# Kernel tuning notes

Hardware: AMD Instinct MI355X
Metric: run time of the kernel (lower is better)

The kernel has to match this reference:

```python
import jax, jax.numpy as jnp
import numpy as np

NUM_COMPONENTS = 8   # component ids 1..8 present; 0 = background (excluded, as in ids[ids>0])
SMOOTH = 1e-5


def setup_inputs() -> dict:
    key = jax.random.key(0)
    k1, k2, k3 = jax.random.split(key, 3)
    B, H, W, D = 2, 160, 160, 160
    y_pred = jax.random.normal(k1, (B, 2, H, W, D), dtype=jnp.float32)
    y = jax.random.randint(k2, (B, 1, H, W, D), 0, 2).astype(jnp.int64)
    components = jax.random.randint(k3, (B, H, W, D), 0, NUM_COMPONENTS + 1).astype(jnp.int64)
    return {"y_pred": y_pred, "y": y, "components": components}


def _soft_dice_loss(inter, psum, tsum):
    # metric(masked_pred, masked_true, mask) = 1 - 2*sum(p*t)/(sum(p)+sum(t)), smoothed
    return 1.0 - (2.0 * inter + SMOOTH) / (psum + tsum + SMOOTH)


def reference(y_pred, y, components):
    # activation: softmax over channel dim 1 (binary logits)
    probs = jax.nn.softmax(y_pred, axis=1)                       # [B,2,H,W,D]
    # one-hot encode int labels -> [B,2,H,W,D] float
    true = jax.nn.one_hot(y[:, 0], y_pred.shape[1], axis=1, dtype=probs.dtype)
    B = probs.shape[0]
    V = components.shape[1] * components.shape[2] * components.shape[3]
    comp = components.reshape(B, V)
    # per-voxel channel-summed quantities (mask-multiply then reduce == segment reduce)
    pp = (probs * true).sum(axis=1).reshape(B, V)                # sum_c p*t
    sp = probs.sum(axis=1).reshape(B, V)                         # sum_c p
    st = true.sum(axis=1).reshape(B, V)                          # sum_c t
    cnt = jnp.ones((B, V), dtype=probs.dtype)

    def seg(d):
        return jax.vmap(lambda dd, cc: jax.ops.segment_sum(dd, cc, num_segments=NUM_COMPONENTS + 1))(d, comp)

    inter, psum, tsum, counts = seg(pp), seg(sp), seg(st), seg(cnt)
    # drop background (component id 0), as torch loops only over ids > 0
    inter, psum, tsum, counts = inter[:, 1:], psum[:, 1:], tsum[:, 1:], counts[:, 1:]
    dice = _soft_dice_loss(inter, psum, tsum)                    # [B, K]
    present = (counts > 0).astype(dice.dtype)                    # only ids in torch.unique
    per_sample = (dice * present).sum(axis=1) / jnp.maximum(present.sum(axis=1), 1.0)
    return per_sample.mean()
```

## Files before the change

kernel.cpp:

```cpp
#include <hip/hip_runtime.h>

#define NB 2
#define NCK 8
#define NVAL (NCK * 2)
#define NBINS (NB * NVAL)
#define SMOOTHF 1e-5f
#define MAXBLK 2048

__global__ __launch_bounds__(256) void cc_accum(
        const float* __restrict__ y_pred,
        const int* __restrict__ y,
        const int* __restrict__ comp,
        float* __restrict__ partial,
        int V4, int half, int nblk) {
    const int b   = (blockIdx.x >= half) ? 1 : 0;
    const int blk = blockIdx.x - b * half;
    const int stride = half * 256;

    float acc[NVAL];
    #pragma unroll
    for (int i = 0; i < NVAL; ++i) acc[i] = 0.0f;

    const float* p0 = y_pred + (long long)b * 2 * ((long long)V4 * 4);
    const float* p1 = p0 + (long long)V4 * 4;
    const int4* yq = (const int4*)y    + (long long)b * V4;
    const int4* cq = (const int4*)comp + (long long)b * V4;

    for (int v = blk * 256 + threadIdx.x; v < V4; v += stride) {
        const float4 a0 = *(const float4*)(p0 + (long long)v * 4);
        const float4 a1 = *(const float4*)(p1 + (long long)v * 4);
        const int4 t = yq[v];
        const int4 c = cq[v];

        {
            float d = a0.x - a1.x;
            float p = 1.0f / (1.0f + __expf(t.x ? d : -d));
            #pragma unroll
            for (int j = 0; j < NCK; ++j) {
                float m = (c.x == j + 1) ? 1.0f : 0.0f;
                acc[2 * j] = fmaf(m, p, acc[2 * j]);
                acc[2 * j + 1] += m;
            }
        }
        {
            float d = a0.y - a1.y;
            float p = 1.0f / (1.0f + __expf(t.y ? d : -d));
            #pragma unroll
            for (int j = 0; j < NCK; ++j) {
                float m = (c.y == j + 1) ? 1.0f : 0.0f;
                acc[2 * j] = fmaf(m, p, acc[2 * j]);
                acc[2 * j + 1] += m;
            }
        }
        {
            float d = a0.z - a1.z;
            float p = 1.0f / (1.0f + __expf(t.z ? d : -d));
            #pragma unroll
            for (int j = 0; j < NCK; ++j) {
                float m = (c.z == j + 1) ? 1.0f : 0.0f;
                acc[2 * j] = fmaf(m, p, acc[2 * j]);
                acc[2 * j + 1] += m;
            }
        }
        {
            float d = a0.w - a1.w;
            float p = 1.0f / (1.0f + __expf(t.w ? d : -d));
            #pragma unroll
            for (int j = 0; j < NCK; ++j) {
                float m = (c.w == j + 1) ? 1.0f : 0.0f;
                acc[2 * j] = fmaf(m, p, acc[2 * j]);
                acc[2 * j + 1] += m;
            }
        }
    }

    #pragma unroll
    for (int i = 0; i < NVAL; ++i) {
        float s = acc[i];
        #pragma unroll
        for (int off = 32; off; off >>= 1) s += __shfl_xor(s, off);
        acc[i] = s;
    }

    __shared__ float red[4][NVAL];
    const int lane = threadIdx.x & 63, wid = threadIdx.x >> 6;
    if (lane == 0) {
        #pragma unroll
        for (int i = 0; i < NVAL; ++i) red[wid][i] = acc[i];
    }
    __syncthreads();
    if (threadIdx.x < NVAL) {
        float s = red[0][threadIdx.x] + red[1][threadIdx.x] +
                  red[2][threadIdx.x] + red[3][threadIdx.x];
        partial[(size_t)(b * NVAL + threadIdx.x) * nblk + blockIdx.x] = s;
    }
}

__global__ __launch_bounds__(256) void cc_reduce(
        const float* __restrict__ partial, float* __restrict__ fin,
        int half, int nblk) {
    const int bin = blockIdx.x;
    const int b = (bin >= NVAL) ? 1 : 0;
    const int c0 = b * half;
    float s = 0.0f;
    for (int i = threadIdx.x; i < half; i += 256)
        s += partial[(size_t)bin * nblk + c0 + i];
    #pragma unroll
    for (int off = 32; off; off >>= 1) s += __shfl_xor(s, off);
    __shared__ float w4[4];
    if ((threadIdx.x & 63) == 0) w4[threadIdx.x >> 6] = s;
    __syncthreads();
    if (threadIdx.x == 0) fin[bin] = w4[0] + w4[1] + w4[2] + w4[3];
}

__global__ void cc_final(const float* __restrict__ fin, float* __restrict__ out) {
    float total = 0.0f;
    for (int b = 0; b < NB; ++b) {
        float dsum = 0.0f, pcount = 0.0f;
        for (int j = 0; j < NCK; ++j) {
            float inter = fin[b * NVAL + 2 * j];
            float cnt   = fin[b * NVAL + 2 * j + 1];
            if (cnt > 0.0f) {
                float dice = 1.0f - (2.0f * inter + SMOOTHF) / (2.0f * cnt + SMOOTHF);
                dsum += dice;
                pcount += 1.0f;
            }
        }
        total += dsum / fmaxf(pcount, 1.0f);
    }
    out[0] = total / (float)NB;
}

extern "C" void kernel_launch(void* const* d_in, const int* in_sizes, int n_in,
                              void* d_out, int out_size, void* d_ws, size_t ws_size,
                              hipStream_t stream) {
    const float* y_pred = (const float*)d_in[0];
    const int*   y      = (const int*)d_in[1];
    const int*   comp   = (const int*)d_in[2];
    float* out = (float*)d_out;
    float* ws  = (float*)d_ws;

    const int nvox = in_sizes[1];
    const int V    = nvox / NB;
    const int V4   = V / 4;

    int half = MAXBLK / 2;
    int need = (V4 + 255) / 256;
    if (half > need) half = need;
    int cap = (int)((ws_size / sizeof(float) - NBINS) / NBINS / 2);
    if (half > cap) half = cap;
    if (half < 1) half = 1;
    const int nblk = 2 * half;

    float* fin = ws + (size_t)NBINS * nblk;

    cc_accum<<<dim3(nblk), dim3(256), 0, stream>>>(y_pred, y, comp, ws, V4, half, nblk);
    cc_reduce<<<dim3(NBINS), dim3(256), 0, stream>>>(ws, fin, half, nblk);
    cc_final<<<dim3(1), dim3(1), 0, stream>>>(fin, out);
}
```

Baseline: 33.97 us.

## Fuse reduction kernels into one finisher and use contiguous per-block chunks with batched loads

The two trailing kernels (per-bin reduce and single-thread final) are merged into one 256-thread finisher that sums row-major per-block partials, which removes a launch. The accumulation kernel now gives each block a contiguous chunk of voxels instead of a grid-strided range. Each thread issues two voxel-quads of loads before computing on them, to raise memory-level parallelism. Out-of-range lanes are handled with clamped indices and a zeroed component mask. The cost is a different partial layout and a single-block final reduction over all partials.

```diff
diff --git a/kernel.cpp b/kernel.cpp
--- a/kernel.cpp
+++ b/kernel.cpp
@@ -3,74 +3,70 @@
 #define NB 2
 #define NCK 8
 #define NVAL (NCK * 2)
-#define NBINS (NB * NVAL)
+#define NSL 32
 #define SMOOTHF 1e-5f
-#define MAXBLK 2048
+
+#define PROC(A0, A1, T, C) do { \
+    float d_ = (A0) - (A1); \
+    float p_ = 1.0f / (1.0f + __expf((T) ? d_ : -d_)); \
+    _Pragma("unroll") \
+    for (int j_ = 0; j_ < NCK; ++j_) { \
+        float m_ = ((C) == j_ + 1) ? 1.0f : 0.0f; \
+        acc[2 * j_] = fmaf(m_, p_, acc[2 * j_]); \
+        acc[2 * j_ + 1] += m_; \
+    } } while (0)
 
 __global__ __launch_bounds__(256) void cc_accum(
         const float* __restrict__ y_pred,
         const int* __restrict__ y,
         const int* __restrict__ comp,
         float* __restrict__ partial,
-        int V4, int half, int nblk) {
-    const int b   = (blockIdx.x >= half) ? 1 : 0;
-    const int blk = blockIdx.x - b * half;
-    const int stride = half * 256;
+        int V4, int BPB, int QB) {
+    const int b   = (blockIdx.x >= BPB) ? 1 : 0;
+    const int blk = blockIdx.x - b * BPB;
+
+    const float* p0 = y_pred + (size_t)b * 2 * ((size_t)V4 * 4);
+    const float* p1 = p0 + (size_t)V4 * 4;
+    const int4* yq = (const int4*)y    + (size_t)b * V4;
+    const int4* cq = (const int4*)comp + (size_t)b * V4;
 
     float acc[NVAL];
     #pragma unroll
     for (int i = 0; i < NVAL; ++i) acc[i] = 0.0f;
 
-    const float* p0 = y_pred + (long long)b * 2 * ((long long)V4 * 4);
-    const float* p1 = p0 + (long long)V4 * 4;
-    const int4* yq = (const int4*)y    + (long long)b * V4;
-    const int4* cq = (const int4*)comp + (long long)b * V4;
+    int vend = blk * QB + QB;
+    if (vend > V4) vend = V4;
+    const int v0 = blk * QB + threadIdx.x;
 
-    for (int v = blk * 256 + threadIdx.x; v < V4; v += stride) {
-        const float4 a0 = *(const float4*)(p0 + (long long)v * 4);
-        const float4 a1 = *(const float4*)(p1 + (long long)v * 4);
-        const int4 t = yq[v];
-        const int4 c = cq[v];
+    for (int base = 0; base < QB; base += 1024) {
+        #pragma unroll
+        for (int k = 0; k < 4; k += 2) {
+            int va = v0 + base + k * 256;
+            int vb = va + 256;
+            const bool ma = va < vend, mb = vb < vend;
+            const int vca = ma ? va : (vend - 1);
+            const int vcb = mb ? vb : (vend - 1);
 
-        {
-            float d = a0.x - a1.x;
-            float p = 1.0f / (1.0f + __expf(t.x ? d : -d));
-            #pragma unroll
-            for (int j = 0; j < NCK; ++j) {
-                float m = (c.x == j + 1) ? 1.0f : 0.0f;
-                acc[2 * j] = fmaf(m, p, acc[2 * j]);
-                acc[2 * j + 1] += m;
-            }
-        }
-        {
-            float d = a0.y - a1.y;
-            float p = 1.0f / (1.0f + __expf(t.y ? d : -d));
-            #pragma unroll
-            for (int j = 0; j < NCK; ++j) {
-                float m = (c.y == j + 1) ? 1.0f : 0.0f;
-                acc[2 * j] = fmaf(m, p, acc[2 * j]);
-                acc[2 * j + 1] += m;
-            }
-        }
-        {
-            float d = a0.z - a1.z;
-            float p = 1.0f / (1.0f + __expf(t.z ? d : -d));
-            #pragma unroll
-            for (int j = 0; j < NCK; ++j) {
-                float m = (c.z == j + 1) ? 1.0f : 0.0f;
-                acc[2 * j] = fmaf(m, p, acc[2 * j]);
-                acc[2 * j + 1] += m;
-            }
-        }
-        {
-            float d = a0.w - a1.w;
-            float p = 1.0f / (1.0f + __expf(t.w ? d : -d));
-            #pragma unroll
-            for (int j = 0; j < NCK; ++j) {
-                float m = (c.w == j + 1) ? 1.0f : 0.0f;
-                acc[2 * j] = fmaf(m, p, acc[2 * j]);
-                acc[2 * j + 1] += m;
-            }
+            const float4 a0a = ((const float4*)p0)[vca];
+            const float4 a1a = ((const float4*)p1)[vca];
+            int4 ta = yq[vca];
+            int4 ca = cq[vca];
+            const float4 a0b = ((const float4*)p0)[vcb];
+            const float4 a1b = ((const float4*)p1)[vcb];
+            int4 tb = yq[vcb];
+            int4 cb = cq[vcb];
+
+            if (!ma) { ca.x = 0; ca.y = 0; ca.z = 0; ca.w = 0; }
+            if (!mb) { cb.x = 0; cb.y = 0; cb.z = 0; cb.w = 0; }
+
+            PROC(a0a.x, a1a.x, ta.x, ca.x);
+            PROC(a0a.y, a1a.y, ta.y, ca.y);
+            PROC(a0a.z, a1a.z, ta.z, ca.z);
+            PROC(a0a.w, a1a.w, ta.w, ca.w);
+            PROC(a0b.x, a1b.x, tb.x, cb.x);
+            PROC(a0b.y, a1b.y, tb.y, cb.y);
+            PROC(a0b.z, a1b.z, tb.z, cb.z);
+            PROC(a0b.w, a1b.w, tb.w, cb.w);
         }
     }
 
@@ -89,46 +85,56 @@
         for (int i = 0; i < NVAL; ++i) red[wid][i] = acc[i];
     }
     __syncthreads();
-    if (threadIdx.x < NVAL) {
-        float s = red[0][threadIdx.x] + red[1][threadIdx.x] +
-                  red[2][threadIdx.x] + red[3][threadIdx.x];
-        partial[(size_t)(b * NVAL + threadIdx.x) * nblk + blockIdx.x] = s;
+    if (threadIdx.x < NSL) {
+        const int j = threadIdx.x;
+        const int jb = j >> 4, jv = j & 15;
+        float s = 0.0f;
+        if (jb == b) s = red[0][jv] + red[1][jv] + red[2][jv] + red[3][jv];
+        partial[(size_t)blockIdx.x * NSL + j] = s;
     }
 }
 
-__global__ __launch_bounds__(256) void cc_reduce(
-        const float* __restrict__ partial, float* __restrict__ fin,
-        int half, int nblk) {
-    const int bin = blockIdx.x;
-    const int b = (bin >= NVAL) ? 1 : 0;
-    const int c0 = b * half;
-    float s = 0.0f;
-    for (int i = threadIdx.x; i < half; i += 256)
-        s += partial[(size_t)bin * nblk + c0 + i];
-    #pragma unroll
-    for (int off = 32; off; off >>= 1) s += __shfl_xor(s, off);
-    __shared__ float w4[4];
-    if ((threadIdx.x & 63) == 0) w4[threadIdx.x >> 6] = s;
+__global__ __launch_bounds__(256) void cc_finish(
+        const float* __restrict__ partial, float* __restrict__ out, int nblk) {
+    float4 a = make_float4(0.f, 0.f, 0.f, 0.f);
+    const float4* p4 = (const float4*)partial;
+    const int nf = nblk * (NSL / 4);
+    for (int f = threadIdx.x; f < nf; f += 256) {
+        const float4 v = p4[f];
+        a.x += v.x; a.y += v.y; a.z += v.z; a.w += v.w;
+    }
+    __shared__ float red[256][4];
+    red[threadIdx.x][0] = a.x;
+    red[threadIdx.x][1] = a.y;
+    red[threadIdx.x][2] = a.z;
+    red[threadIdx.x][3] = a.w;
     __syncthreads();
-    if (threadIdx.x == 0) fin[bin] = w4[0] + w4[1] + w4[2] + w4[3];
-}
-
-__global__ void cc_final(const float* __restrict__ fin, float* __restrict__ out) {
-    float total = 0.0f;
-    for (int b = 0; b < NB; ++b) {
-        float dsum = 0.0f, pcount = 0.0f;
-        for (int j = 0; j < NCK; ++j) {
-            float inter = fin[b * NVAL + 2 * j];
-            float cnt   = fin[b * NVAL + 2 * j + 1];
-            if (cnt > 0.0f) {
-                float dice = 1.0f - (2.0f * inter + SMOOTHF) / (2.0f * cnt + SMOOTHF);
-                dsum += dice;
-                pcount += 1.0f;
+    __shared__ float fin[NSL];
+    if (threadIdx.x < NSL) {
+        const int c = threadIdx.x;
+        const int grp = c >> 2, k = c & 3;
+        float s = 0.0f;
+        #pragma unroll 8
+        for (int g = 0; g < 32; ++g) s += red[g * 8 + grp][k];
+        fin[c] = s;
+    }
+    __syncthreads();
+    if (threadIdx.x == 0) {
+        float total = 0.0f;
+        for (int b = 0; b < NB; ++b) {
+            float dsum = 0.0f, pc = 0.0f;
+            for (int j = 0; j < NCK; ++j) {
+                const float inter = fin[b * NVAL + 2 * j];
+                const float cnt   = fin[b * NVAL + 2 * j + 1];
+                if (cnt > 0.0f) {
+                    dsum += 1.0f - (2.0f * inter + SMOOTHF) / (2.0f * cnt + SMOOTHF);
+                    pc += 1.0f;
+                }
             }
+            total += dsum / fmaxf(pc, 1.0f);
         }
-        total += dsum / fmaxf(pcount, 1.0f);
+        out[0] = total / (float)NB;
     }
-    out[0] = total / (float)NB;
 }
 
 extern "C" void kernel_launch(void* const* d_in, const int* in_sizes, int n_in,
@@ -144,17 +150,14 @@
     const int V    = nvox / NB;
     const int V4   = V / 4;
 
-    int half = MAXBLK / 2;
-    int need = (V4 + 255) / 256;
-    if (half > need) half = need;
-    int cap = (int)((ws_size / sizeof(float) - NBINS) / NBINS / 2);
-    if (half > cap) half = cap;
-    if (half < 1) half = 1;
-    const int nblk = 2 * half;
+    int BPB = 1024;
+    int cap_rows = (int)(ws_size / (NSL * sizeof(float)));
+    if (2 * BPB > cap_rows) BPB = cap_rows / 2;
+    if (BPB > V4) BPB = V4;
+    if (BPB < 1) BPB = 1;
+    const int QB = (V4 + BPB - 1) / BPB;
+    const int nblk = 2 * BPB;
 
-    float* fin = ws + (size_t)NBINS * nblk;
-
-    cc_accum<<<dim3(nblk), dim3(256), 0, stream>>>(y_pred, y, comp, ws, V4, half, nblk);
-    cc_reduce<<<dim3(NBINS), dim3(256), 0, stream>>>(ws, fin, half, nblk);
-    cc_final<<<dim3(1), dim3(1), 0, stream>>>(fin, out);
+    cc_accum<<<dim3(nblk), dim3(256), 0, stream>>>(y_pred, y, comp, ws, V4, BPB, QB);
+    cc_finish<<<dim3(1), dim3(256), 0, stream>>>(ws, out, nblk);
 }
```

New measurement: 45.57 us. 1.34x slower.
